# Kernel optimization log

Measured on AMD Instinct MI355X. Metric: run time of the kernel, lower is better.

Reference implementation:

```python
import jax, jax.numpy as jnp
import numpy as np

N_DRUG = 50000
N_GENE = 50000
E = 600000
D_IN = 128
D_HID = 64
D_EMB = 32


def setup_inputs() -> dict:
    key = jax.random.key(0)
    ks = jax.random.split(key, 32)
    inp = {}
    inp['x_drug'] = jax.random.normal(ks[0], (N_DRUG, D_IN), jnp.float32)
    inp['x_gene'] = jax.random.normal(ks[1], (N_GENE, D_IN), jnp.float32)
    # per-etype edge lists (src,dst)
    inp['dd_src'] = jax.random.randint(ks[2], (E,), 0, N_DRUG)
    inp['dd_dst'] = jax.random.randint(ks[3], (E,), 0, N_DRUG)
    inp['dg_src'] = jax.random.randint(ks[4], (E,), 0, N_DRUG)
    inp['dg_dst'] = jax.random.randint(ks[5], (E,), 0, N_GENE)
    inp['gd_src'] = jax.random.randint(ks[6], (E,), 0, N_GENE)
    inp['gd_dst'] = jax.random.randint(ks[7], (E,), 0, N_DRUG)
    inp['gg_src'] = jax.random.randint(ks[8], (E,), 0, N_GENE)
    inp['gg_dst'] = jax.random.randint(ks[9], (E,), 0, N_GENE)
    # layer-1 per-relation weights (in -> hidden) and per-ntype biases
    s1 = 1.0 / np.sqrt(D_IN)
    inp['W1_dd'] = jax.random.normal(ks[10], (D_IN, D_HID), jnp.float32) * s1
    inp['W1_dg'] = jax.random.normal(ks[11], (D_IN, D_HID), jnp.float32) * s1
    inp['W1_gd'] = jax.random.normal(ks[12], (D_IN, D_HID), jnp.float32) * s1
    inp['W1_gg'] = jax.random.normal(ks[13], (D_IN, D_HID), jnp.float32) * s1
    inp['b1_drug'] = jnp.zeros((D_HID,), jnp.float32)
    inp['b1_gene'] = jnp.zeros((D_HID,), jnp.float32)
    # layer-2 per-relation weights (hidden -> embed) and per-ntype biases
    s2 = 1.0 / np.sqrt(D_HID)
    inp['W2_dd'] = jax.random.normal(ks[14], (D_HID, D_EMB), jnp.float32) * s2
    inp['W2_dg'] = jax.random.normal(ks[15], (D_HID, D_EMB), jnp.float32) * s2
    inp['W2_gd'] = jax.random.normal(ks[16], (D_HID, D_EMB), jnp.float32) * s2
    inp['W2_gg'] = jax.random.normal(ks[17], (D_HID, D_EMB), jnp.float32) * s2
    inp['b2_drug'] = jnp.zeros((D_EMB,), jnp.float32)
    inp['b2_gene'] = jnp.zeros((D_EMB,), jnp.float32)
    return inp


def _rel_mean(x_src, W, src, dst, n_dst):
    # transform-then-gather (efficient when out_dim <= in_dim), segment-mean over dst
    m = (x_src @ W)[src]                                  # [E, out]
    s = jax.ops.segment_sum(m, dst, num_segments=n_dst)   # [n_dst, out]
    deg = jax.ops.segment_sum(jnp.ones((src.shape[0],), m.dtype), dst, num_segments=n_dst)
    return s / jnp.maximum(deg, 1.0)[:, None]


def _rgcn_layer(xd, xg, Wdd, Wdg, Wgd, Wgg, bd, bg,
                dd_src, dd_dst, dg_src, dg_dst, gd_src, gd_dst, gg_src, gg_dst, act):
    hd = (_rel_mean(xd, Wdd, dd_src, dd_dst, N_DRUG)
          + _rel_mean(xg, Wgd, gd_src, gd_dst, N_DRUG) + bd)
    hg = (_rel_mean(xd, Wdg, dg_src, dg_dst, N_GENE)
          + _rel_mean(xg, Wgg, gg_src, gg_dst, N_GENE) + bg)
    if act:
        hd = jax.nn.relu(hd)
        hg = jax.nn.relu(hg)
    return hd, hg


def reference(x_drug, x_gene, dd_src, dd_dst, dg_src, dg_dst, gd_src, gd_dst,
              gg_src, gg_dst, W1_dd, W1_dg, W1_gd, W1_gg, b1_drug, b1_gene,
              W2_dd, W2_dg, W2_gd, W2_gg, b2_drug, b2_gene):
    hd, hg = _rgcn_layer(x_drug, x_gene, W1_dd, W1_dg, W1_gd, W1_gg, b1_drug, b1_gene,
                         dd_src, dd_dst, dg_src, dg_dst, gd_src, gd_dst, gg_src, gg_dst, True)
    hd, hg = _rgcn_layer(hd, hg, W2_dd, W2_dg, W2_gd, W2_gg, b2_drug, b2_gene,
                         dd_src, dd_dst, dg_src, dg_dst, gd_src, gd_dst, gg_src, gg_dst, False)
    # concatenate per-ntype embeddings: rows [0:N_DRUG]=drug, [N_DRUG:]=gene
    return jnp.concatenate([hd, hg], axis=0)
```

## Files before the change

### kernel.cpp

```cpp
#include <hip/hip_runtime.h>
#include <hip/hip_bf16.h>

#define N_NODE 50000
#define NEDGE  600000
#define NRANGE 128
#define RSZ    391
#define CAPB   6144
#define CHUNK  4096
#define NBLK1  147

typedef __hip_bfloat16 bf16;
typedef __attribute__((ext_vector_type(8))) short short8;
typedef __attribute__((ext_vector_type(4))) float floatx4;

__device__ __forceinline__ short f2s(float f) {
    bf16 t = __float2bfloat16(f);
    return *(short*)&t;
}
__device__ __forceinline__ unsigned pk2(float lo, float hi) {
    return ((unsigned)(unsigned short)f2s(lo)) | (((unsigned)(unsigned short)f2s(hi)) << 16);
}
__device__ __forceinline__ void acc2(float& a, float& b, unsigned w, float m) {
    a += m * __uint_as_float(w << 16);
    b += m * __uint_as_float(w & 0xFFFF0000u);
}


__global__ __launch_bounds__(256) void k_part(
    const int* __restrict__ d0, const int* __restrict__ s0,
    const int* __restrict__ d1, const int* __restrict__ s1,
    const int* __restrict__ d2, const int* __restrict__ s2,
    const int* __restrict__ d3, const int* __restrict__ s3,
    int* __restrict__ gcur, unsigned* __restrict__ gpart)
{
    __shared__ int hcur[NRANGE];
    __shared__ int delta[NRANGE];
    __shared__ int sc[256];
    __shared__ unsigned buf[CHUNK];
    int bid = blockIdx.x;
    int rel = bid / NBLK1;
    int c   = bid - rel * NBLK1;
    int tid = threadIdx.x;
    const int* dp = rel == 0 ? d0 : rel == 1 ? d1 : rel == 2 ? d2 : d3;
    const int* sp = rel == 0 ? s0 : rel == 1 ? s1 : rel == 2 ? s2 : s3;
    int e0 = c * CHUNK;
    int e1 = min(e0 + CHUNK, NEDGE);
    int cnt_chunk = e1 - e0;

    if (tid < NRANGE) hcur[tid] = 0;
    __syncthreads();
    for (int e = e0 + tid; e < e1; e += 256)
        atomicAdd(&hcur[dp[e] / RSZ], 1);
    __syncthreads();
    int v = (tid < NRANGE) ? hcur[tid] : 0;
    sc[tid] = v;
    __syncthreads();
    for (int d = 1; d < NRANGE; d <<= 1) {
        int t = (tid >= d && tid < NRANGE) ? sc[tid - d] : 0;
        __syncthreads();
        sc[tid] += t;
        __syncthreads();
    }
    if (tid < NRANGE) {
        int start = sc[tid] - v;
        int bg    = rel * NRANGE + tid;
        int resv  = atomicAdd(&gcur[bg], v);
        delta[tid] = bg * CAPB + resv - start;
        hcur[tid]  = start;
    }
    __syncthreads();
    for (int e = e0 + tid; e < e1; e += 256) {
        int d = dp[e];
        int b = d / RSZ;
        int p = atomicAdd(&hcur[b], 1);
        buf[p] = ((unsigned)b << 25) | ((unsigned)(d - b * RSZ) << 16) | (unsigned)sp[e];
    }
    __syncthreads();
    for (int i = tid; i < cnt_chunk; i += 256) {
        unsigned key = buf[i];
        gpart[delta[key >> 25] + i] = key;
    }
}

__global__ __launch_bounds__(512) void k_base(
    const int* __restrict__ gcur, int* __restrict__ base_rel)
{
    __shared__ int sc[512];
    int t = threadIdx.x;
    int v = gcur[t];
    sc[t] = v;
    __syncthreads();
    int loc = t & (NRANGE - 1);
    for (int d = 1; d < NRANGE; d <<= 1) {
        int x = (loc >= d) ? sc[t - d] : 0;
        __syncthreads();
        sc[t] += x;
        __syncthreads();
    }
    base_rel[t] = sc[t] - v;
}

__global__ __launch_bounds__(256) void k_csr(
    const unsigned* __restrict__ gpart, const int* __restrict__ gcnt,
    const int* __restrict__ base_rel, int* __restrict__ off, int* __restrict__ edges)
{
    __shared__ int cur[RSZ];
    __shared__ unsigned short stg[CAPB];
    __shared__ int sc[256];
    int bid = blockIdx.x;
    int rel = bid >> 7, r = bid & (NRANGE - 1);
    int tid = threadIdx.x;
    int range0 = r * RSZ;
    int RS = min(RSZ, N_NODE - range0);
    if (RS < 0) RS = 0;
    int count = gcnt[bid];
    int base  = base_rel[bid];
    size_t slot0 = (size_t)bid * CAPB;

    for (int i = tid; i < RSZ; i += 256) cur[i] = 0;
    __syncthreads();
    for (int i = tid; i < count; i += 256)
        atomicAdd(&cur[(gpart[slot0 + i] >> 16) & 0x1FF], 1);
    __syncthreads();
    int vloc[2]; int run = 0;
#pragma unroll
    for (int j = 0; j < 2; j++) {
        int idx = tid * 2 + j;
        int x = (idx < RSZ) ? cur[idx] : 0;
        vloc[j] = x; run += x;
    }
    sc[tid] = run;
    __syncthreads();
    for (int d = 1; d < 256; d <<= 1) {
        int t = (tid >= d) ? sc[tid - d] : 0;
        __syncthreads();
        sc[tid] += t;
        __syncthreads();
    }
    int excl = sc[tid] - run;
    run = excl;
#pragma unroll
    for (int j = 0; j < 2; j++) {
        int idx = tid * 2 + j;
        if (idx < RSZ) { int x = vloc[j]; cur[idx] = run; run += x; }
    }
    __syncthreads();
    for (int i = tid; i < RS; i += 256)
        off[rel * (N_NODE + 1) + range0 + i] = base + cur[i];
    if (r == NRANGE - 1 && tid == 0) off[rel * (N_NODE + 1) + N_NODE] = NEDGE;
    __syncthreads();
    for (int i = tid; i < count; i += 256) {
        unsigned key = gpart[slot0 + i];
        int p = atomicAdd(&cur[(key >> 16) & 0x1FF], 1);
        stg[p] = (unsigned short)(key & 0xFFFFu);
    }
    __syncthreads();
    for (int i = tid; i < count; i += 256)
        edges[rel * NEDGE + base + i] = (int)stg[i];
}

template <int K, int NOUT, bool AFP32>
__global__ __launch_bounds__(256) void k_gemm_pair(
    const void* __restrict__ X0, const void* __restrict__ X1,
    const float* __restrict__ Wa0, const float* __restrict__ Wb0,
    const float* __restrict__ Wa1, const float* __restrict__ Wb1,
    bf16* __restrict__ out0, bf16* __restrict__ out1, int M)
{
    constexpr int NB  = NOUT / 16;
    constexpr int KC  = K / 32;
    constexpr int NH  = NOUT / 2;
    constexpr int NBL = (NB == 8) ? 3 : 2;
    __shared__ short Wl[KC * NB * 512];

    int sel = blockIdx.y;
    const void*  X  = sel ? X1 : X0;
    const float* Wa = sel ? Wa1 : Wa0;
    const float* Wb = sel ? Wb1 : Wb0;
    bf16*        out = sel ? out1 : out0;

    int tid = threadIdx.x;
    for (int i = tid; i < KC * NB * 512; i += 256) {
        int j  = i & 7;
        int n  = (i >> 3) & 15;
        int q  = (i >> 7) & 3;
        int nb = (i >> 9) & (NB - 1);
        int kc = i >> (9 + NBL);
        int k  = kc * 32 + q * 8 + j;
        int c  = nb * 16 + n;
        float w = (c < NH) ? Wa[k * NH + c] : Wb[k * NH + (c - NH)];
        Wl[i] = f2s(w);
    }
    __syncthreads();

    int lane = tid & 63, wv = tid >> 6;
    int q = lane >> 4, lidx = lane & 15;
    int row0 = blockIdx.x * 64 + wv * 16;
    int rowA = min(row0 + lidx, M - 1);

    floatx4 acc[NB];
#pragma unroll
    for (int nb = 0; nb < NB; nb++) acc[nb] = (floatx4){0.f, 0.f, 0.f, 0.f};

#pragma unroll
    for (int kc = 0; kc < KC; kc++) {
        short8 a;
        if constexpr (AFP32) {
            const float* Xf = (const float*)X + (size_t)rowA * K + kc * 32 + q * 8;
            float4 f0 = *(const float4*)Xf;
            float4 f1 = *(const float4*)(Xf + 4);
            a[0] = f2s(f0.x); a[1] = f2s(f0.y); a[2] = f2s(f0.z); a[3] = f2s(f0.w);
            a[4] = f2s(f1.x); a[5] = f2s(f1.y); a[6] = f2s(f1.z); a[7] = f2s(f1.w);
        } else {
            a = *(const short8*)((const short*)X + (size_t)rowA * K + kc * 32 + q * 8);
        }
#pragma unroll
        for (int nb = 0; nb < NB; nb++) {
            short8 b = *(const short8*)&Wl[((kc * NB + nb) * 64 + lane) * 8];
            acc[nb] = __builtin_amdgcn_mfma_f32_16x16x32_bf16(a, b, acc[nb], 0, 0, 0);
        }
    }
#pragma unroll
    for (int nb = 0; nb < NB; nb++) {
#pragma unroll
        for (int r = 0; r < 4; r++) {
            int row = row0 + q * 4 + r;
            if (row < M)
                out[(size_t)row * NOUT + nb * 16 + lidx] = __float2bfloat16(acc[nb][r]);
        }
    }
}

template<int ROWU>
__device__ __forceinline__ void seg_run(
    int n, const int* __restrict__ ep, float sc,
    const unsigned* __restrict__ base, float* s)
{
    int nfull = n & ~3;
    for (int i = 0; i < nfull; i += 4) {
        int e0 = ep[i + 0];
        int e1 = ep[i + 1];
        int e2 = ep[i + 2];
        int e3 = ep[i + 3];
        uint4 w0 = *(const uint4*)(base + e0 * ROWU);
        uint4 w1 = *(const uint4*)(base + e1 * ROWU);
        uint4 w2 = *(const uint4*)(base + e2 * ROWU);
        uint4 w3 = *(const uint4*)(base + e3 * ROWU);
        acc2(s[0], s[1], w0.x, sc); acc2(s[2], s[3], w0.y, sc);
        acc2(s[4], s[5], w0.z, sc); acc2(s[6], s[7], w0.w, sc);
        acc2(s[0], s[1], w1.x, sc); acc2(s[2], s[3], w1.y, sc);
        acc2(s[4], s[5], w1.z, sc); acc2(s[6], s[7], w1.w, sc);
        acc2(s[0], s[1], w2.x, sc); acc2(s[2], s[3], w2.y, sc);
        acc2(s[4], s[5], w2.z, sc); acc2(s[6], s[7], w2.w, sc);
        acc2(s[0], s[1], w3.x, sc); acc2(s[2], s[3], w3.y, sc);
        acc2(s[4], s[5], w3.z, sc); acc2(s[6], s[7], w3.w, sc);
    }
    for (int i = nfull; i < n; i++) {
        int e = ep[i];
        uint4 w = *(const uint4*)(base + e * ROWU);
        acc2(s[0], s[1], w.x, sc); acc2(s[2], s[3], w.y, sc);
        acc2(s[4], s[5], w.z, sc); acc2(s[6], s[7], w.w, sc);
    }
}

__global__ __launch_bounds__(256) void k_gather64v2(
    const bf16* __restrict__ m1,
    const int* __restrict__ offA0, const int* __restrict__ eA0,
    const int* __restrict__ offB0, const int* __restrict__ eB0,
    const float* __restrict__ bias0, bf16* __restrict__ out0,
    const int* __restrict__ offA1, const int* __restrict__ eA1,
    const int* __restrict__ offB1, const int* __restrict__ eB1,
    const float* __restrict__ bias1, bf16* __restrict__ out1)
{
    int tid  = threadIdx.x;
    int gid  = blockIdx.x * 32 + (tid >> 3);
    int lidx = tid & 7;
    int half = (gid >= N_NODE);
    int wid  = gid - (half ? N_NODE : 0);
    const int* offA = half ? offA1 : offA0;
    const int* eA   = half ? eA1   : eA0;
    const int* offB = half ? offB1 : offB0;
    const int* eB   = half ? eB1   : eB0;
    const float* bias = half ? bias1 : bias0;
    bf16* out = half ? out1 : out0;

    const unsigned* base = (const unsigned*)m1 + (half ? 32 : 0) + lidx * 4;

    int begA = offA[wid], nA = offA[wid + 1] - begA;
    int begB = offB[wid], nB = offB[wid + 1] - begB;
    float ia = 1.f / (float)max(nA, 1);
    float ib = 1.f / (float)max(nB, 1);

    float s[8] = {0.f,0.f,0.f,0.f,0.f,0.f,0.f,0.f};
    seg_run<64>(nA, eA + begA, ia, base, s);
    seg_run<64>(nB, eB + begB, ib, base + N_NODE * 64, s);

    float h[8];
#pragma unroll
    for (int k = 0; k < 8; k++)
        h[k] = fmaxf(s[k] + bias[lidx * 8 + k], 0.f);
    uint4 v;
    v.x = pk2(h[0], h[1]); v.y = pk2(h[2], h[3]);
    v.z = pk2(h[4], h[5]); v.w = pk2(h[6], h[7]);
    *(uint4*)(out + (size_t)wid * 64 + lidx * 8) = v;
}

__global__ __launch_bounds__(256) void k_gather32v2(
    const bf16* __restrict__ m2,
    const int* __restrict__ offA0, const int* __restrict__ eA0,
    const int* __restrict__ offB0, const int* __restrict__ eB0,
    const float* __restrict__ bias0, float* __restrict__ out0,
    const int* __restrict__ offA1, const int* __restrict__ eA1,
    const int* __restrict__ offB1, const int* __restrict__ eB1,
    const float* __restrict__ bias1, float* __restrict__ out1)
{
    int tid  = threadIdx.x;
    int gid  = blockIdx.x * 64 + (tid >> 2);
    int lidx = tid & 3;
    if (gid >= 2 * N_NODE) return;
    int half = (gid >= N_NODE);
    int wid  = gid - (half ? N_NODE : 0);
    const int* offA = half ? offA1 : offA0;
    const int* eA   = half ? eA1   : eA0;
    const int* offB = half ? offB1 : offB0;
    const int* eB   = half ? eB1   : eB0;
    const float* bias = half ? bias1 : bias0;
    float* out = half ? out1 : out0;

    const unsigned* base = (const unsigned*)m2 + (half ? 16 : 0) + lidx * 4;

    int begA = offA[wid], nA = offA[wid + 1] - begA;
    int begB = offB[wid], nB = offB[wid + 1] - begB;
    float ia = 1.f / (float)max(nA, 1);
    float ib = 1.f / (float)max(nB, 1);

    float s[8] = {0.f,0.f,0.f,0.f,0.f,0.f,0.f,0.f};
    seg_run<32>(nA, eA + begA, ia, base, s);
    seg_run<32>(nB, eB + begB, ib, base + N_NODE * 32, s);

    float* o = out + (size_t)wid * 32 + lidx * 8;
    float4 v0, v1;
    v0.x = s[0] + bias[lidx * 8 + 0];
    v0.y = s[1] + bias[lidx * 8 + 1];
    v0.z = s[2] + bias[lidx * 8 + 2];
    v0.w = s[3] + bias[lidx * 8 + 3];
    v1.x = s[4] + bias[lidx * 8 + 4];
    v1.y = s[5] + bias[lidx * 8 + 5];
    v1.z = s[6] + bias[lidx * 8 + 6];
    v1.w = s[7] + bias[lidx * 8 + 7];
    *(float4*)o = v0;
    *(float4*)(o + 4) = v1;
}

extern "C" void kernel_launch(void* const* d_in, const int* in_sizes, int n_in,
                              void* d_out, int out_size, void* d_ws, size_t ws_size,
                              hipStream_t stream)
{
    const float* xd = (const float*)d_in[0];
    const float* xg = (const float*)d_in[1];
    const int* dd_src = (const int*)d_in[2];  const int* dd_dst = (const int*)d_in[3];
    const int* dg_src = (const int*)d_in[4];  const int* dg_dst = (const int*)d_in[5];
    const int* gd_src = (const int*)d_in[6];  const int* gd_dst = (const int*)d_in[7];
    const int* gg_src = (const int*)d_in[8];  const int* gg_dst = (const int*)d_in[9];
    const float* W1dd = (const float*)d_in[10];
    const float* W1dg = (const float*)d_in[11];
    const float* W1gd = (const float*)d_in[12];
    const float* W1gg = (const float*)d_in[13];
    const float* b1d  = (const float*)d_in[14];
    const float* b1g  = (const float*)d_in[15];
    const float* W2dd = (const float*)d_in[16];
    const float* W2dg = (const float*)d_in[17];
    const float* W2gd = (const float*)d_in[18];
    const float* W2gg = (const float*)d_in[19];
    const float* b2d  = (const float*)d_in[20];
    const float* b2g  = (const float*)d_in[21];
    float* out = (float*)d_out;

    int* gcur     = (int*)d_ws;
    int* base_rel = gcur + 512;
    int* off      = base_rel + 512;
    int* edges    = off + 4 * (N_NODE + 1);
    bf16* md1     = (bf16*)(edges + 4 * NEDGE);
    bf16* mg1     = md1 + (size_t)N_NODE * 128;
    bf16* hd      = mg1 + (size_t)N_NODE * 128;
    bf16* hg      = hd + (size_t)N_NODE * 64;
    bf16* md2     = md1;
    bf16* mg2     = md1 + (size_t)N_NODE * 64;
    unsigned* gpart = (unsigned*)md1;

    hipMemsetAsync(gcur, 0, 512 * sizeof(int), stream);
    k_part<<<4 * NBLK1, 256, 0, stream>>>(
        dd_dst, dd_src, gd_dst, gd_src, dg_dst, dg_src, gg_dst, gg_src, gcur, gpart);
    k_base<<<1, 512, 0, stream>>>(gcur, base_rel);
    k_csr<<<512, 256, 0, stream>>>(gpart, gcur, base_rel, off, edges);

    const int* off_dd = off + 0 * (N_NODE + 1);
    const int* off_gd = off + 1 * (N_NODE + 1);
    const int* off_dg = off + 2 * (N_NODE + 1);
    const int* off_gg = off + 3 * (N_NODE + 1);
    const int* e_dd = edges + 0 * NEDGE;
    const int* e_gd = edges + 1 * NEDGE;
    const int* e_dg = edges + 2 * NEDGE;
    const int* e_gg = edges + 3 * NEDGE;

    dim3 gemm_grid((N_NODE + 63) / 64, 2);
    int g64_grid = (2 * N_NODE) / 32;
    int g32_grid = (2 * N_NODE + 63) / 64;

    k_gemm_pair<128, 128, true><<<gemm_grid, 256, 0, stream>>>(
        xd, xg, W1dd, W1dg, W1gd, W1gg, md1, mg1, N_NODE);
    k_gather64v2<<<g64_grid, 256, 0, stream>>>(
        md1,
        off_dd, e_dd, off_gd, e_gd, b1d, hd,
        off_dg, e_dg, off_gg, e_gg, b1g, hg);

    k_gemm_pair<64, 64, false><<<gemm_grid, 256, 0, stream>>>(
        hd, hg, W2dd, W2dg, W2gd, W2gg, md2, mg2, N_NODE);
    k_gather32v2<<<g32_grid, 256, 0, stream>>>(
        md2,
        off_dd, e_dd, off_gd, e_gd, b2d, out,
        off_dg, e_dg, off_gg, e_gg, b2g, out + (size_t)N_NODE * 32);
}
```

Measured before the change: 338.5 us.

## Merge partition with layer-1 GEMM, 16-bit edges, gather-then-transform layer 2

```diff
diff --git a/kernel.cpp b/kernel.cpp
--- a/kernel.cpp
+++ b/kernel.cpp
@@ -8,6 +8,7 @@
 #define CAPB   6144
 #define CHUNK  4096
 #define NBLK1  147
+#define GEMM_GX 782
 
 typedef __hip_bfloat16 bf16;
 typedef __attribute__((ext_vector_type(8))) short short8;
@@ -26,83 +27,127 @@
 }
 
 
-__global__ __launch_bounds__(256) void k_part(
+__global__ __launch_bounds__(256) void k_part_gemm(
     const int* __restrict__ d0, const int* __restrict__ s0,
     const int* __restrict__ d1, const int* __restrict__ s1,
     const int* __restrict__ d2, const int* __restrict__ s2,
     const int* __restrict__ d3, const int* __restrict__ s3,
-    int* __restrict__ gcur, unsigned* __restrict__ gpart)
-{
-    __shared__ int hcur[NRANGE];
-    __shared__ int delta[NRANGE];
-    __shared__ int sc[256];
-    __shared__ unsigned buf[CHUNK];
-    int bid = blockIdx.x;
-    int rel = bid / NBLK1;
-    int c   = bid - rel * NBLK1;
+    int* __restrict__ gcur, unsigned* __restrict__ gpart,
+    const float* __restrict__ X0, const float* __restrict__ X1,
+    const float* __restrict__ Wa0, const float* __restrict__ Wb0,
+    const float* __restrict__ Wa1, const float* __restrict__ Wb1,
+    bf16* __restrict__ out0, bf16* __restrict__ out1)
+{
+    __shared__ union {
+        struct { int hcur[NRANGE]; int delta[NRANGE]; int sc[256]; unsigned buf[CHUNK]; } p;
+        short wl[4 * 8 * 512];
+    } u;
+
     int tid = threadIdx.x;
-    const int* dp = rel == 0 ? d0 : rel == 1 ? d1 : rel == 2 ? d2 : d3;
-    const int* sp = rel == 0 ? s0 : rel == 1 ? s1 : rel == 2 ? s2 : s3;
-    int e0 = c * CHUNK;
-    int e1 = min(e0 + CHUNK, NEDGE);
-    int cnt_chunk = e1 - e0;
-
-    if (tid < NRANGE) hcur[tid] = 0;
-    __syncthreads();
-    for (int e = e0 + tid; e < e1; e += 256)
-        atomicAdd(&hcur[dp[e] / RSZ], 1);
-    __syncthreads();
-    int v = (tid < NRANGE) ? hcur[tid] : 0;
-    sc[tid] = v;
-    __syncthreads();
-    for (int d = 1; d < NRANGE; d <<= 1) {
-        int t = (tid >= d && tid < NRANGE) ? sc[tid - d] : 0;
-        __syncthreads();
-        sc[tid] += t;
-        __syncthreads();
-    }
-    if (tid < NRANGE) {
-        int start = sc[tid] - v;
-        int bg    = rel * NRANGE + tid;
-        int resv  = atomicAdd(&gcur[bg], v);
-        delta[tid] = bg * CAPB + resv - start;
-        hcur[tid]  = start;
-    }
-    __syncthreads();
-    for (int e = e0 + tid; e < e1; e += 256) {
-        int d = dp[e];
-        int b = d / RSZ;
-        int p = atomicAdd(&hcur[b], 1);
-        buf[p] = ((unsigned)b << 25) | ((unsigned)(d - b * RSZ) << 16) | (unsigned)sp[e];
-    }
-    __syncthreads();
-    for (int i = tid; i < cnt_chunk; i += 256) {
-        unsigned key = buf[i];
-        gpart[delta[key >> 25] + i] = key;
-    }
-}
-
-__global__ __launch_bounds__(512) void k_base(
-    const int* __restrict__ gcur, int* __restrict__ base_rel)
-{
-    __shared__ int sc[512];
-    int t = threadIdx.x;
-    int v = gcur[t];
-    sc[t] = v;
-    __syncthreads();
-    int loc = t & (NRANGE - 1);
-    for (int d = 1; d < NRANGE; d <<= 1) {
-        int x = (loc >= d) ? sc[t - d] : 0;
-        __syncthreads();
-        sc[t] += x;
-        __syncthreads();
-    }
-    base_rel[t] = sc[t] - v;
+    if (blockIdx.x < 4 * NBLK1) {
+        int bid = blockIdx.x;
+        int rel = bid / NBLK1;
+        int c   = bid - rel * NBLK1;
+        const int* dp = rel == 0 ? d0 : rel == 1 ? d1 : rel == 2 ? d2 : d3;
+        const int* sp = rel == 0 ? s0 : rel == 1 ? s1 : rel == 2 ? s2 : s3;
+        int e0 = c * CHUNK;
+        int e1 = min(e0 + CHUNK, NEDGE);
+        int cnt_chunk = e1 - e0;
+
+        if (tid < NRANGE) u.p.hcur[tid] = 0;
+        __syncthreads();
+        for (int e = e0 + tid; e < e1; e += 256)
+            atomicAdd(&u.p.hcur[dp[e] / RSZ], 1);
+        __syncthreads();
+        int v = (tid < NRANGE) ? u.p.hcur[tid] : 0;
+        u.p.sc[tid] = v;
+        __syncthreads();
+        for (int d = 1; d < NRANGE; d <<= 1) {
+            int t = (tid >= d && tid < NRANGE) ? u.p.sc[tid - d] : 0;
+            __syncthreads();
+            u.p.sc[tid] += t;
+            __syncthreads();
+        }
+        if (tid < NRANGE) {
+            int start = u.p.sc[tid] - v;
+            int bg    = rel * NRANGE + tid;
+            int resv  = atomicAdd(&gcur[bg], v);
+            u.p.delta[tid] = bg * CAPB + resv - start;
+            u.p.hcur[tid]  = start;
+        }
+        __syncthreads();
+        for (int e = e0 + tid; e < e1; e += 256) {
+            int d = dp[e];
+            int b = d / RSZ;
+            int p = atomicAdd(&u.p.hcur[b], 1);
+            u.p.buf[p] = ((unsigned)b << 25) | ((unsigned)(d - b * RSZ) << 16) | (unsigned)sp[e];
+        }
+        __syncthreads();
+        for (int i = tid; i < cnt_chunk; i += 256) {
+            unsigned key = u.p.buf[i];
+            gpart[u.p.delta[key >> 25] + i] = key;
+        }
+    } else {
+        constexpr int NB = 8, KC = 4, NH = 64;
+        int bid2 = blockIdx.x - 4 * NBLK1;
+        int sel  = bid2 >= GEMM_GX;
+        int bx   = sel ? bid2 - GEMM_GX : bid2;
+        const float* X  = sel ? X1 : X0;
+        const float* Wa = sel ? Wa1 : Wa0;
+        const float* Wb = sel ? Wb1 : Wb0;
+        bf16*       outp = sel ? out1 : out0;
+
+        for (int i = tid; i < KC * NB * 512; i += 256) {
+            int j  = i & 7;
+            int n  = (i >> 3) & 15;
+            int q  = (i >> 7) & 3;
+            int nb = (i >> 9) & (NB - 1);
+            int kc = i >> 12;
+            int k  = kc * 32 + q * 8 + j;
+            int c  = nb * 16 + n;
+            float w = (c < NH) ? Wa[k * NH + c] : Wb[k * NH + (c - NH)];
+            u.wl[i] = f2s(w);
+        }
+        __syncthreads();
+
+        int lane = tid & 63, wv = tid >> 6;
+        int q = lane >> 4, lidx = lane & 15;
+        int row0 = bx * 64 + wv * 16;
+        int rowA = min(row0 + lidx, N_NODE - 1);
+
+        floatx4 acc[NB];
+#pragma unroll
+        for (int nb = 0; nb < NB; nb++) acc[nb] = (floatx4){0.f, 0.f, 0.f, 0.f};
+
+#pragma unroll
+        for (int kc = 0; kc < KC; kc++) {
+            const float* Xf = X + (size_t)rowA * 128 + kc * 32 + q * 8;
+            float4 f0 = *(const float4*)Xf;
+            float4 f1 = *(const float4*)(Xf + 4);
+            short8 a;
+            a[0] = f2s(f0.x); a[1] = f2s(f0.y); a[2] = f2s(f0.z); a[3] = f2s(f0.w);
+            a[4] = f2s(f1.x); a[5] = f2s(f1.y); a[6] = f2s(f1.z); a[7] = f2s(f1.w);
+#pragma unroll
+            for (int nb = 0; nb < NB; nb++) {
+                short8 b = *(const short8*)&u.wl[((kc * NB + nb) * 64 + lane) * 8];
+                acc[nb] = __builtin_amdgcn_mfma_f32_16x16x32_bf16(a, b, acc[nb], 0, 0, 0);
+            }
+        }
+#pragma unroll
+        for (int nb = 0; nb < NB; nb++) {
+#pragma unroll
+            for (int r = 0; r < 4; r++) {
+                int row = row0 + q * 4 + r;
+                if (row < N_NODE)
+                    outp[(size_t)row * 128 + nb * 16 + lidx] = __float2bfloat16(acc[nb][r]);
+            }
+        }
+    }
 }
 
 __global__ __launch_bounds__(256) void k_csr(
     const unsigned* __restrict__ gpart, const int* __restrict__ gcnt,
-    const int* __restrict__ base_rel, int* __restrict__ off, int* __restrict__ edges)
+    int* __restrict__ off, unsigned short* __restrict__ edges)
 {
     __shared__ int cur[RSZ];
     __shared__ unsigned short stg[CAPB];
@@ -114,8 +159,19 @@
     int RS = min(RSZ, N_NODE - range0);
     if (RS < 0) RS = 0;
     int count = gcnt[bid];
-    int base  = base_rel[bid];
     size_t slot0 = (size_t)bid * CAPB;
+
+    int vb = (tid < NRANGE) ? gcnt[rel * NRANGE + tid] : 0;
+    sc[tid] = vb;
+    __syncthreads();
+    for (int d = 1; d < NRANGE; d <<= 1) {
+        int t = (tid >= d && tid < NRANGE) ? sc[tid - d] : 0;
+        __syncthreads();
+        sc[tid] += t;
+        __syncthreads();
+    }
+    int base = (r > 0) ? sc[r - 1] : 0;
+    __syncthreads();
 
     for (int i = tid; i < RSZ; i += 256) cur[i] = 0;
     __syncthreads();
@@ -156,83 +212,12 @@
     }
     __syncthreads();
     for (int i = tid; i < count; i += 256)
-        edges[rel * NEDGE + base + i] = (int)stg[i];
-}
-
-template <int K, int NOUT, bool AFP32>
-__global__ __launch_bounds__(256) void k_gemm_pair(
-    const void* __restrict__ X0, const void* __restrict__ X1,
-    const float* __restrict__ Wa0, const float* __restrict__ Wb0,
-    const float* __restrict__ Wa1, const float* __restrict__ Wb1,
-    bf16* __restrict__ out0, bf16* __restrict__ out1, int M)
-{
-    constexpr int NB  = NOUT / 16;
-    constexpr int KC  = K / 32;
-    constexpr int NH  = NOUT / 2;
-    constexpr int NBL = (NB == 8) ? 3 : 2;
-    __shared__ short Wl[KC * NB * 512];
-
-    int sel = blockIdx.y;
-    const void*  X  = sel ? X1 : X0;
-    const float* Wa = sel ? Wa1 : Wa0;
-    const float* Wb = sel ? Wb1 : Wb0;
-    bf16*        out = sel ? out1 : out0;
-
-    int tid = threadIdx.x;
-    for (int i = tid; i < KC * NB * 512; i += 256) {
-        int j  = i & 7;
-        int n  = (i >> 3) & 15;
-        int q  = (i >> 7) & 3;
-        int nb = (i >> 9) & (NB - 1);
-        int kc = i >> (9 + NBL);
-        int k  = kc * 32 + q * 8 + j;
-        int c  = nb * 16 + n;
-        float w = (c < NH) ? Wa[k * NH + c] : Wb[k * NH + (c - NH)];
-        Wl[i] = f2s(w);
-    }
-    __syncthreads();
-
-    int lane = tid & 63, wv = tid >> 6;
-    int q = lane >> 4, lidx = lane & 15;
-    int row0 = blockIdx.x * 64 + wv * 16;
-    int rowA = min(row0 + lidx, M - 1);
-
-    floatx4 acc[NB];
-#pragma unroll
-    for (int nb = 0; nb < NB; nb++) acc[nb] = (floatx4){0.f, 0.f, 0.f, 0.f};
-
-#pragma unroll
-    for (int kc = 0; kc < KC; kc++) {
-        short8 a;
-        if constexpr (AFP32) {
-            const float* Xf = (const float*)X + (size_t)rowA * K + kc * 32 + q * 8;
-            float4 f0 = *(const float4*)Xf;
-            float4 f1 = *(const float4*)(Xf + 4);
-            a[0] = f2s(f0.x); a[1] = f2s(f0.y); a[2] = f2s(f0.z); a[3] = f2s(f0.w);
-            a[4] = f2s(f1.x); a[5] = f2s(f1.y); a[6] = f2s(f1.z); a[7] = f2s(f1.w);
-        } else {
-            a = *(const short8*)((const short*)X + (size_t)rowA * K + kc * 32 + q * 8);
-        }
-#pragma unroll
-        for (int nb = 0; nb < NB; nb++) {
-            short8 b = *(const short8*)&Wl[((kc * NB + nb) * 64 + lane) * 8];
-            acc[nb] = __builtin_amdgcn_mfma_f32_16x16x32_bf16(a, b, acc[nb], 0, 0, 0);
-        }
-    }
-#pragma unroll
-    for (int nb = 0; nb < NB; nb++) {
-#pragma unroll
-        for (int r = 0; r < 4; r++) {
-            int row = row0 + q * 4 + r;
-            if (row < M)
-                out[(size_t)row * NOUT + nb * 16 + lidx] = __float2bfloat16(acc[nb][r]);
-        }
-    }
+        edges[(size_t)rel * NEDGE + base + i] = stg[i];
 }
 
 template<int ROWU>
 __device__ __forceinline__ void seg_run(
-    int n, const int* __restrict__ ep, float sc,
+    int n, const unsigned short* __restrict__ ep, float sc,
     const unsigned* __restrict__ base, float* s)
 {
     int nfull = n & ~3;
@@ -262,13 +247,13 @@
     }
 }
 
-__global__ __launch_bounds__(256) void k_gather64v2(
+__global__ __launch_bounds__(256) void k_gather64v5(
     const bf16* __restrict__ m1,
-    const int* __restrict__ offA0, const int* __restrict__ eA0,
-    const int* __restrict__ offB0, const int* __restrict__ eB0,
+    const int* __restrict__ offA0, const unsigned short* __restrict__ eA0,
+    const int* __restrict__ offB0, const unsigned short* __restrict__ eB0,
     const float* __restrict__ bias0, bf16* __restrict__ out0,
-    const int* __restrict__ offA1, const int* __restrict__ eA1,
-    const int* __restrict__ offB1, const int* __restrict__ eB1,
+    const int* __restrict__ offA1, const unsigned short* __restrict__ eA1,
+    const int* __restrict__ offB1, const unsigned short* __restrict__ eB1,
     const float* __restrict__ bias1, bf16* __restrict__ out1)
 {
     int tid  = threadIdx.x;
@@ -277,9 +262,9 @@
     int half = (gid >= N_NODE);
     int wid  = gid - (half ? N_NODE : 0);
     const int* offA = half ? offA1 : offA0;
-    const int* eA   = half ? eA1   : eA0;
+    const unsigned short* eA = half ? eA1 : eA0;
     const int* offB = half ? offB1 : offB0;
-    const int* eB   = half ? eB1   : eB0;
+    const unsigned short* eB = half ? eB1 : eB0;
     const float* bias = half ? bias1 : bias0;
     bf16* out = half ? out1 : out0;
 
@@ -304,51 +289,68 @@
     *(uint4*)(out + (size_t)wid * 64 + lidx * 8) = v;
 }
 
-__global__ __launch_bounds__(256) void k_gather32v2(
-    const bf16* __restrict__ m2,
-    const int* __restrict__ offA0, const int* __restrict__ eA0,
-    const int* __restrict__ offB0, const int* __restrict__ eB0,
-    const float* __restrict__ bias0, float* __restrict__ out0,
-    const int* __restrict__ offA1, const int* __restrict__ eA1,
-    const int* __restrict__ offB1, const int* __restrict__ eB1,
-    const float* __restrict__ bias1, float* __restrict__ out1)
-{
+__global__ __launch_bounds__(256) void k_gather32ft(
+    const bf16* __restrict__ h,
+    const int* __restrict__ off, const unsigned short* __restrict__ edges,
+    const float* __restrict__ W2dd, const float* __restrict__ W2gd,
+    const float* __restrict__ W2dg, const float* __restrict__ W2gg,
+    const float* __restrict__ b2d, const float* __restrict__ b2g,
+    float* __restrict__ out)
+{
+    __shared__ float hb[32][2][66];
     int tid  = threadIdx.x;
-    int gid  = blockIdx.x * 64 + (tid >> 2);
-    int lidx = tid & 3;
-    if (gid >= 2 * N_NODE) return;
+    int grp  = tid >> 3;
+    int lidx = tid & 7;
+    int gid  = blockIdx.x * 32 + grp;
     int half = (gid >= N_NODE);
     int wid  = gid - (half ? N_NODE : 0);
-    const int* offA = half ? offA1 : offA0;
-    const int* eA   = half ? eA1   : eA0;
-    const int* offB = half ? offB1 : offB0;
-    const int* eB   = half ? eB1   : eB0;
-    const float* bias = half ? bias1 : bias0;
-    float* out = half ? out1 : out0;
-
-    const unsigned* base = (const unsigned*)m2 + (half ? 16 : 0) + lidx * 4;
+    const int* offA = off + (half ? 2 : 0) * (N_NODE + 1);
+    const int* offB = off + (half ? 3 : 1) * (N_NODE + 1);
+    const unsigned short* eA = edges + (size_t)(half ? 2 : 0) * NEDGE;
+    const unsigned short* eB = edges + (size_t)(half ? 3 : 1) * NEDGE;
+
+    const unsigned* base = (const unsigned*)h + lidx * 4;
 
     int begA = offA[wid], nA = offA[wid + 1] - begA;
     int begB = offB[wid], nB = offB[wid + 1] - begB;
     float ia = 1.f / (float)max(nA, 1);
     float ib = 1.f / (float)max(nB, 1);
 
-    float s[8] = {0.f,0.f,0.f,0.f,0.f,0.f,0.f,0.f};
-    seg_run<32>(nA, eA + begA, ia, base, s);
-    seg_run<32>(nB, eB + begB, ib, base + N_NODE * 32, s);
-
-    float* o = out + (size_t)wid * 32 + lidx * 8;
-    float4 v0, v1;
-    v0.x = s[0] + bias[lidx * 8 + 0];
-    v0.y = s[1] + bias[lidx * 8 + 1];
-    v0.z = s[2] + bias[lidx * 8 + 2];
-    v0.w = s[3] + bias[lidx * 8 + 3];
-    v1.x = s[4] + bias[lidx * 8 + 4];
-    v1.y = s[5] + bias[lidx * 8 + 5];
-    v1.z = s[6] + bias[lidx * 8 + 6];
-    v1.w = s[7] + bias[lidx * 8 + 7];
-    *(float4*)o = v0;
-    *(float4*)(o + 4) = v1;
+    float sA[8] = {0.f,0.f,0.f,0.f,0.f,0.f,0.f,0.f};
+    float sB[8] = {0.f,0.f,0.f,0.f,0.f,0.f,0.f,0.f};
+    seg_run<32>(nA, eA + begA, ia, base, sA);
+    seg_run<32>(nB, eB + begB, ib, base + N_NODE * 32, sB);
+
+#pragma unroll
+    for (int k = 0; k < 8; k++) {
+        hb[grp][0][lidx * 8 + k] = sA[k];
+        hb[grp][1][lidx * 8 + k] = sB[k];
+    }
+    __syncthreads();
+
+    const float* Wa = half ? W2dg : W2dd;
+    const float* Wb = half ? W2gg : W2gd;
+    const float* bias = half ? b2g : b2d;
+    const float* hbA = hb[grp][0];
+    const float* hbB = hb[grp][1];
+    int j0 = lidx * 4;
+    float o0 = 0.f, o1 = 0.f, o2 = 0.f, o3 = 0.f;
+#pragma unroll 8
+    for (int k = 0; k < 64; k++) {
+        float a = hbA[k], b = hbB[k];
+        float4 wa = *(const float4*)(Wa + k * 32 + j0);
+        float4 wb = *(const float4*)(Wb + k * 32 + j0);
+        o0 += a * wa.x + b * wb.x;
+        o1 += a * wa.y + b * wb.y;
+        o2 += a * wa.z + b * wb.z;
+        o3 += a * wa.w + b * wb.w;
+    }
+    float4 v;
+    v.x = o0 + bias[j0 + 0];
+    v.y = o1 + bias[j0 + 1];
+    v.z = o2 + bias[j0 + 2];
+    v.w = o3 + bias[j0 + 3];
+    *(float4*)(out + (size_t)gid * 32 + j0) = v;
 }
 
 extern "C" void kernel_launch(void* const* d_in, const int* in_sizes, int n_in,
@@ -376,47 +378,36 @@
     float* out = (float*)d_out;
 
     int* gcur     = (int*)d_ws;
-    int* base_rel = gcur + 512;
-    int* off      = base_rel + 512;
-    int* edges    = off + 4 * (N_NODE + 1);
-    bf16* md1     = (bf16*)(edges + 4 * NEDGE);
+    int* off      = gcur + 512;
+    unsigned short* edges = (unsigned short*)(off + 4 * (N_NODE + 1));
+    bf16* md1     = (bf16*)(edges + (size_t)4 * NEDGE);
     bf16* mg1     = md1 + (size_t)N_NODE * 128;
-    bf16* hd      = mg1 + (size_t)N_NODE * 128;
-    bf16* hg      = hd + (size_t)N_NODE * 64;
-    bf16* md2     = md1;
-    bf16* mg2     = md1 + (size_t)N_NODE * 64;
-    unsigned* gpart = (unsigned*)md1;
+    bf16* h       = mg1 + (size_t)N_NODE * 128;
+    unsigned* gpart = (unsigned*)h;
 
     hipMemsetAsync(gcur, 0, 512 * sizeof(int), stream);
-    k_part<<<4 * NBLK1, 256, 0, stream>>>(
-        dd_dst, dd_src, gd_dst, gd_src, dg_dst, dg_src, gg_dst, gg_src, gcur, gpart);
-    k_base<<<1, 512, 0, stream>>>(gcur, base_rel);
-    k_csr<<<512, 256, 0, stream>>>(gpart, gcur, base_rel, off, edges);
+    k_part_gemm<<<4 * NBLK1 + 2 * GEMM_GX, 256, 0, stream>>>(
+        dd_dst, dd_src, gd_dst, gd_src, dg_dst, dg_src, gg_dst, gg_src, gcur, gpart,
+        xd, xg, W1dd, W1dg, W1gd, W1gg, md1, mg1);
+
+    k_csr<<<512, 256, 0, stream>>>(gpart, gcur, off, edges);
 
     const int* off_dd = off + 0 * (N_NODE + 1);
     const int* off_gd = off + 1 * (N_NODE + 1);
     const int* off_dg = off + 2 * (N_NODE + 1);
     const int* off_gg = off + 3 * (N_NODE + 1);
-    const int* e_dd = edges + 0 * NEDGE;
-    const int* e_gd = edges + 1 * NEDGE;
-    const int* e_dg = edges + 2 * NEDGE;
-    const int* e_gg = edges + 3 * NEDGE;
-
-    dim3 gemm_grid((N_NODE + 63) / 64, 2);
-    int g64_grid = (2 * N_NODE) / 32;
-    int g32_grid = (2 * N_NODE + 63) / 64;
-
-    k_gemm_pair<128, 128, true><<<gemm_grid, 256, 0, stream>>>(
-        xd, xg, W1dd, W1dg, W1gd, W1gg, md1, mg1, N_NODE);
-    k_gather64v2<<<g64_grid, 256, 0, stream>>>(
+    const unsigned short* e_dd = edges + (size_t)0 * NEDGE;
+    const unsigned short* e_gd = edges + (size_t)1 * NEDGE;
+    const unsigned short* e_dg = edges + (size_t)2 * NEDGE;
+    const unsigned short* e_gg = edges + (size_t)3 * NEDGE;
+
+    int g_grid = (2 * N_NODE) / 32;
+
+    k_gather64v5<<<g_grid, 256, 0, stream>>>(
         md1,
-        off_dd, e_dd, off_gd, e_gd, b1d, hd,
-        off_dg, e_dg, off_gg, e_gg, b1g, hg);
-
-    k_gemm_pair<64, 64, false><<<gemm_grid, 256, 0, stream>>>(
-        hd, hg, W2dd, W2dg, W2gd, W2gg, md2, mg2, N_NODE);
-    k_gather32v2<<<g32_grid, 256, 0, stream>>>(
-        md2,
-        off_dd, e_dd, off_gd, e_gd, b2d, out,
-        off_dg, e_dg, off_gg, e_gg, b2g, out + (size_t)N_NODE * 32);
-}
+        off_dd, e_dd, off_gd, e_gd, b1d, h,
+        off_dg, e_dg, off_gg, e_gg, b1g, h + (size_t)N_NODE * 64);
+
+    k_gather32ft<<<g_grid, 256, 0, stream>>>(
+        h, off, edges, W2dd, W2gd, W2dg, W2gg, b2d, b2g, out);
+}
```

Result: slower. 345.9 us (+2.2%).
